# Optimization experiments

Measured on AMD Instinct MI355X. Metric: run time of the kernel, lower is better.

## Reference

```python
import jax, jax.numpy as jnp
import numpy as np

EMBED_DIM = 1024
NUM_HEADS = 16
HEAD_DIM = EMBED_DIM // NUM_HEADS
B, S = 4, 2048


def setup_inputs() -> dict:
    key = jax.random.key(0)
    ks = jax.random.split(key, 9)
    s = 1.0 / np.sqrt(EMBED_DIM)
    x = jax.random.normal(ks[0], (B, S, EMBED_DIM), dtype=jnp.float32)
    # nn.Linear weights stored [out, in]; y = x @ W.T + b
    Wq = jax.random.uniform(ks[1], (EMBED_DIM, EMBED_DIM), jnp.float32, -s, s)
    bq = jax.random.uniform(ks[2], (EMBED_DIM,), jnp.float32, -s, s)
    Wk = jax.random.uniform(ks[3], (EMBED_DIM, EMBED_DIM), jnp.float32, -s, s)
    bk = jax.random.uniform(ks[4], (EMBED_DIM,), jnp.float32, -s, s)
    Wv = jax.random.uniform(ks[5], (EMBED_DIM, EMBED_DIM), jnp.float32, -s, s)
    bv = jax.random.uniform(ks[6], (EMBED_DIM,), jnp.float32, -s, s)
    Wo = jax.random.uniform(ks[7], (EMBED_DIM, EMBED_DIM), jnp.float32, -s, s)
    bo = jax.random.uniform(ks[8], (EMBED_DIM,), jnp.float32, -s, s)
    return {"x": x, "Wq": Wq, "bq": bq, "Wk": Wk, "bk": bk,
            "Wv": Wv, "bv": bv, "Wo": Wo, "bo": bo}


def _split_heads(t):
    b, s, _ = t.shape
    return t.reshape(b, s, NUM_HEADS, HEAD_DIM).transpose(0, 2, 1, 3)  # [B,H,S,D]


def reference(x, Wq, bq, Wk, bk, Wv, bv, Wo, bo):
    q = _split_heads(x @ Wq.T + bq)
    k = _split_heads(x @ Wk.T + bk)
    v = _split_heads(x @ Wv.T + bv)
    scores = jnp.einsum('bhqd,bhkd->bhqk', q, k) / np.sqrt(HEAD_DIM)  # [B,H,S,S]
    attn = jax.nn.softmax(scores, axis=-1)
    ctx = jnp.einsum('bhqk,bhkd->bhqd', attn, v)          # [B,H,S,D]
    ctx = ctx.transpose(0, 2, 1, 3).reshape(x.shape[0], x.shape[1], EMBED_DIM)
    return ctx @ Wo.T + bo
```

## Files before the change

kernel.cpp:

```cpp
#include <hip/hip_runtime.h>
#include <hip/hip_bf16.h>
#include <stdint.h>

typedef __attribute__((ext_vector_type(8))) short  bf16x8;
typedef __attribute__((ext_vector_type(4))) float  f32x4;
typedef __attribute__((ext_vector_type(4))) unsigned int u32x4;
typedef __attribute__((ext_vector_type(2))) unsigned int u32x2;

#define LOG2E 1.4426950408889634f

__device__ __forceinline__ unsigned short f2bf(float f) {
  unsigned int u = __builtin_bit_cast(unsigned int, f);
  u += 0x7fffu + ((u >> 16) & 1u);
  return (unsigned short)(u >> 16);
}

__device__ __forceinline__ unsigned int pk2(float a, float b) {
  __hip_bfloat162 h = __float22bfloat162_rn(make_float2(a, b));
  unsigned int u;
  __builtin_memcpy(&u, &h, 4);
  return u;
}

__device__ __forceinline__ void async16(const void* g, void* l) {
  __builtin_amdgcn_global_load_lds(
      (const __attribute__((address_space(1))) unsigned int*)g,
      (__attribute__((address_space(3))) unsigned int*)l,
      16, 0, 0);
}

__global__ __launch_bounds__(256) void cast_all(
    const float* __restrict__ x,
    const float* __restrict__ Wq, const float* __restrict__ Wk,
    const float* __restrict__ Wv, const float* __restrict__ Wo,
    unsigned short* __restrict__ xb, unsigned short* __restrict__ wqkv,
    unsigned short* __restrict__ wo) {
  int i = blockIdx.x * 256 + threadIdx.x;
  const float* src;
  unsigned short* dst;
  int off;
  if (i < 2097152) {
    src = x; dst = xb; off = i;
  } else {
    int j = i - 2097152;
    int seg = j >> 18; off = j & 262143;
    src = (seg == 0) ? Wq : (seg == 1) ? Wk : (seg == 2) ? Wv : Wo;
    dst = (seg < 3) ? (wqkv + (size_t)seg * 1048576) : wo;
  }
  float4 f = ((const float4*)src)[off];
  uint2 o;
  o.x = pk2(f.x, f.y);
  o.y = pk2(f.z, f.w);
  ((uint2*)dst)[off] = o;
}

__global__ __launch_bounds__(256) void gemm_qkv(
    const unsigned short* __restrict__ xb, const unsigned short* __restrict__ wqkv,
    const float* __restrict__ bq, const float* __restrict__ bk, const float* __restrict__ bv,
    unsigned short* __restrict__ qb, unsigned short* __restrict__ kb,
    unsigned short* __restrict__ vb) {
  __shared__ __align__(16) unsigned short As[128 * 32];
  __shared__ __align__(16) unsigned short Bs[128 * 32];
  __shared__ __align__(16) unsigned short epi[4][64 * 72];
  const int bid = blockIdx.x;
  const int xcd = bid & 7, idx = bid >> 3;
  const int nt = xcd * 3 + (idx % 3);
  const int mt = idx / 3;
  const int m0 = mt * 128, n0 = nt * 128;
  const int tid = threadIdx.x;
  const int wv = tid >> 6, lane = tid & 63, qq = lane >> 4, ln = lane & 15;
  const int wm = wv & 1, wn = wv >> 1;
  const int K = 1024;

  f32x4 acc[4][4];
#pragma unroll
  for (int i = 0; i < 4; ++i)
#pragma unroll
    for (int j = 0; j < 4; ++j) acc[i][j] = f32x4{0.f, 0.f, 0.f, 0.f};

  for (int k0 = 0; k0 < K; k0 += 32) {
#pragma unroll
    for (int i = 0; i < 2; ++i) {
      int cc = wv * 2 + i;
      int jp = cc * 64 + lane;
      int row = jp >> 2, cp = jp & 3;
      int c = cp ^ ((row >> 1) & 3);
      async16(xb   + (size_t)(m0 + row) * K + k0 + c * 8, As + cc * 512);
      async16(wqkv + (size_t)(n0 + row) * K + k0 + c * 8, Bs + cc * 512);
    }
    __syncthreads();
    bf16x8 af[4], bf[4];
#pragma unroll
    for (int i = 0; i < 4; ++i) {
      int row = wm * 64 + i * 16 + ln;
      af[i] = *(const bf16x8*)(As + row * 32 + (qq ^ ((row >> 1) & 3)) * 8);
    }
#pragma unroll
    for (int j = 0; j < 4; ++j) {
      int row = wn * 64 + j * 16 + ln;
      bf[j] = *(const bf16x8*)(Bs + row * 32 + (qq ^ ((row >> 1) & 3)) * 8);
    }
#pragma unroll
    for (int i = 0; i < 4; ++i)
#pragma unroll
      for (int j = 0; j < 4; ++j)
        acc[i][j] = __builtin_amdgcn_mfma_f32_16x16x32_bf16(af[i], bf[j], acc[i][j], 0, 0, 0);
    __syncthreads();
  }

  const int nblk = n0 >> 10;
  const float* bias = (nblk == 0) ? bq : (nblk == 1) ? bk : bv;
  const float scale = (nblk == 0) ? (0.125f * LOG2E) : 1.0f;
  unsigned short* buf = epi[wv];
  const int ncol0 = (n0 & 1023) + wn * 64;
  const int head  = ncol0 >> 6;
  const int mbase = m0 + wm * 64;
  const int b     = mbase >> 11, sbase = mbase & 2047;
  unsigned short* dst = (nblk == 0) ? qb : (nblk == 1) ? kb : vb;

  if (nblk != 2) {
#pragma unroll
    for (int j = 0; j < 4; ++j) {
      float bs = bias[ncol0 + j * 16 + ln] * scale;
#pragma unroll
      for (int i = 0; i < 4; ++i)
#pragma unroll
        for (int r = 0; r < 4; ++r)
          buf[(i * 16 + qq * 4 + r) * 72 + j * 16 + ln] = f2bf(acc[i][j][r] * scale + bs);
    }
    unsigned short* gout = dst + (((size_t)(b * 16 + head)) * 2048 + sbase) * 64;
#pragma unroll
    for (int h = 0; h < 2; ++h)
#pragma unroll
      for (int p = 0; p < 4; ++p) {
        int rr = (lane >> 2) + p * 16;
        int c4 = lane & 3;
        ulonglong2 v = *(const ulonglong2*)(buf + rr * 72 + h * 32 + c4 * 8);
        *(ulonglong2*)(gout + (size_t)rr * 64 + h * 32 + c4 * 8) = v;
      }
  } else {
#pragma unroll
    for (int j = 0; j < 4; ++j) {
      float bs = bias[ncol0 + j * 16 + ln];
#pragma unroll
      for (int i = 0; i < 4; ++i) {
        uint2 pk;
        pk.x = pk2(acc[i][j][0] + bs, acc[i][j][1] + bs);
        pk.y = pk2(acc[i][j][2] + bs, acc[i][j][3] + bs);
        *(uint2*)(buf + (j * 16 + ln) * 72 + i * 16 + qq * 4) = pk;
      }
    }
    unsigned short* gout = dst + ((size_t)(b * 16 + head)) * 64 * 2048 + sbase;
#pragma unroll
    for (int p = 0; p < 8; ++p) {
      int dr = (lane >> 3) + p * 8;
      int c8 = lane & 7;
      ulonglong2 v = *(const ulonglong2*)(buf + dr * 72 + c8 * 8);
      *(ulonglong2*)(gout + (size_t)dr * 2048 + c8 * 8) = v;
    }
  }
}

__global__ __launch_bounds__(256, 2) void attn_kernel(
    const unsigned short* __restrict__ qb, const unsigned short* __restrict__ kb,
    const unsigned short* __restrict__ vb, unsigned short* __restrict__ ctx) {
  __shared__ __align__(16) unsigned short sh[16384];
  const int bid = blockIdx.x;
  const int xcd = bid & 7, idx = bid >> 3;
  const int bh = xcd * 8 + (idx >> 3);
  const int q0 = (idx & 7) * 256;
  const int tid = threadIdx.x;
  const int wv = tid >> 6, lane = tid & 63, qq = lane >> 4, ln = lane & 15;

  bf16x8 qf[4][2];
  {
    const unsigned short* qbase = qb + ((size_t)bh * 2048 + q0 + wv * 64) * 64;
#pragma unroll
    for (int rb = 0; rb < 4; ++rb)
#pragma unroll
      for (int kq = 0; kq < 2; ++kq)
        qf[rb][kq] = *(const bf16x8*)(qbase + (rb * 16 + ln) * 64 + kq * 32 + qq * 8);
  }

  f32x4 o_acc[4][4];
  float l_i[4] = {0.f, 0.f, 0.f, 0.f};
#pragma unroll
  for (int rb = 0; rb < 4; ++rb)
#pragma unroll
    for (int nt = 0; nt < 4; ++nt) o_acc[rb][nt] = f32x4{0.f, 0.f, 0.f, 0.f};
  const f32x4 z4 = f32x4{0.f, 0.f, 0.f, 0.f};

  const unsigned short* kgbase = kb + (size_t)bh * 2048 * 64;
  const unsigned short* vgbase = vb + (size_t)bh * 64 * 2048;
  const int cc0 = wv * 2;

  auto stageKV = [&](int kt, int buf) {
#pragma unroll
    for (int i = 0; i < 2; ++i) {
      int jp = (cc0 + i) * 64 + lane;
      int row = jp >> 3, c = (jp & 7) ^ (row & 7);
      async16(kgbase + (size_t)(kt * 64 + row) * 64 + c * 8,
              sh + buf * 4096 + (cc0 + i) * 512);
      async16(vgbase + (size_t)row * 2048 + kt * 64 + c * 8,
              sh + 8192 + buf * 4096 + (cc0 + i) * 512);
    }
  };

  stageKV(0, 0);
  asm volatile("s_waitcnt vmcnt(0)" ::: "memory");
  __builtin_amdgcn_s_barrier();

  for (int kt = 0; kt < 32; ++kt) {
    const int cur = kt & 1;
    const unsigned short* kcur = sh + cur * 4096;
    const unsigned short* vcur = sh + 8192 + cur * 4096;
    if (kt < 31) stageKV(kt + 1, cur ^ 1);

    bf16x8 kf[4][2];
#pragma unroll
    for (int ct = 0; ct < 4; ++ct) {
      int row = ct * 16 + ln;
      kf[ct][0] = *(const bf16x8*)(kcur + row * 64 + ((0 + qq) ^ (row & 7)) * 8);
      kf[ct][1] = *(const bf16x8*)(kcur + row * 64 + ((4 + qq) ^ (row & 7)) * 8);
    }
    bf16x8 vf[2][4];
#pragma unroll
    for (int kk = 0; kk < 2; ++kk)
#pragma unroll
      for (int nt = 0; nt < 4; ++nt) {
        int row = nt * 16 + ln;
        vf[kk][nt] = *(const bf16x8*)(vcur + row * 64 + ((kk * 4 + qq) ^ (row & 7)) * 8);
      }

    auto QK = [&](const bf16x8& q0f, const bf16x8& q1f, f32x4* s) {
#pragma unroll
      for (int ct = 0; ct < 4; ++ct) {
        s[ct] = __builtin_amdgcn_mfma_f32_16x16x32_bf16(kf[ct][0], q0f, z4, 0, 0, 0);
        s[ct] = __builtin_amdgcn_mfma_f32_16x16x32_bf16(kf[ct][1], q1f, s[ct], 0, 0, 0);
      }
    };
    auto SM = [&](float& li, const f32x4* s, bf16x8* pfo) {
      unsigned int W[4][2];
#pragma unroll
      for (int ct = 0; ct < 4; ++ct) {
        float p0 = __builtin_amdgcn_exp2f(s[ct][0]);
        float p1 = __builtin_amdgcn_exp2f(s[ct][1]);
        float p2 = __builtin_amdgcn_exp2f(s[ct][2]);
        float p3 = __builtin_amdgcn_exp2f(s[ct][3]);
        li += (p0 + p1) + (p2 + p3);
        W[ct][0] = pk2(p0, p1);
        W[ct][1] = pk2(p2, p3);
      }
#pragma unroll
      for (int kk = 0; kk < 2; ++kk) {
        u32x2 a1 = __builtin_amdgcn_permlane32_swap(W[2 * kk][0], W[2 * kk + 1][0], false, false);
        u32x2 a2 = __builtin_amdgcn_permlane16_swap(a1.x, a1.y, false, false);
        u32x2 b1 = __builtin_amdgcn_permlane32_swap(W[2 * kk][1], W[2 * kk + 1][1], false, false);
        u32x2 b2 = __builtin_amdgcn_permlane16_swap(b1.x, b1.y, false, false);
        u32x4 pw = {a2.x, b2.x, a2.y, b2.y};
        pfo[kk] = __builtin_bit_cast(bf16x8, pw);
      }
    };
    auto PV = [&](f32x4* oa, const bf16x8* pfi) {
#pragma unroll
      for (int kk = 0; kk < 2; ++kk)
#pragma unroll
        for (int nt = 0; nt < 4; ++nt)
          oa[nt] = __builtin_amdgcn_mfma_f32_16x16x32_bf16(vf[kk][nt], pfi[kk], oa[nt], 0, 0, 0);
    };

    f32x4 s0[4], s1[4], s2[4], s3[4];
    bf16x8 p0[2], p1[2], p2[2], p3[2];
    QK(qf[0][0], qf[0][1], s0);
    QK(qf[1][0], qf[1][1], s1);  SM(l_i[0], s0, p0);
    QK(qf[2][0], qf[2][1], s2);  SM(l_i[1], s1, p1);  PV(o_acc[0], p0);
    QK(qf[3][0], qf[3][1], s3);  SM(l_i[2], s2, p2);  PV(o_acc[1], p1);
                                 SM(l_i[3], s3, p3);  PV(o_acc[2], p2);
                                                      PV(o_acc[3], p3);

    if (kt < 31) asm volatile("s_waitcnt vmcnt(0)" ::: "memory");
    __builtin_amdgcn_s_barrier();
  }

  unsigned short* ep = sh;
#pragma unroll
  for (int rb = 0; rb < 4; ++rb) {
    l_i[rb] += __shfl_xor(l_i[rb], 16);
    l_i[rb] += __shfl_xor(l_i[rb], 32);
    float inv = 1.0f / l_i[rb];
    int row = wv * 64 + rb * 16 + ln;
    int rs = row & 7;
#pragma unroll
    for (int nt = 0; nt < 4; ++nt) {
      uint2 pk;
      pk.x = pk2(o_acc[rb][nt][0] * inv, o_acc[rb][nt][1] * inv);
      pk.y = pk2(o_acc[rb][nt][2] * inv, o_acc[rb][nt][3] * inv);
      *(uint2*)(ep + row * 64 + (((nt * 2 + (qq >> 1)) ^ rs) << 3) + ((qq & 1) << 2)) = pk;
    }
  }
  {
    const int b = bh >> 4, h = bh & 15;
    int r = tid;
    int rs2 = r & 7;
    size_t gbase = ((size_t)(b * 2048 + q0 + r)) * 1024 + h * 64;
    const unsigned short* lsrc = ep + r * 64;
#pragma unroll
    for (int j = 0; j < 8; ++j)
      *(ulonglong2*)(ctx + gbase + (size_t)j * 8) =
          *(const ulonglong2*)(lsrc + ((j ^ rs2) << 3));
  }
}

__global__ __launch_bounds__(256) void gemm_out(
    const unsigned short* __restrict__ ctx, const unsigned short* __restrict__ wo,
    const float* __restrict__ bo, float* __restrict__ out) {
  __shared__ __align__(16) unsigned short As[2][128 * 32];
  __shared__ __align__(16) unsigned short Bs[2][128 * 32];
  const int bid = blockIdx.x;
  const int n0 = (bid & 7) * 128;
  const int m0 = (bid >> 3) * 128;
  const int tid = threadIdx.x;
  const int wv = tid >> 6, lane = tid & 63, qq = lane >> 4, ln = lane & 15;
  const int wm = wv & 1, wn = wv >> 1;
  const int K = 1024;

  f32x4 acc[4][4];
#pragma unroll
  for (int i = 0; i < 4; ++i)
#pragma unroll
    for (int j = 0; j < 4; ++j) acc[i][j] = f32x4{0.f, 0.f, 0.f, 0.f};

  auto stage = [&](int t, int buf) {
#pragma unroll
    for (int i = 0; i < 2; ++i) {
      int cc = wv * 2 + i;
      int jp = cc * 64 + lane;
      int row = jp >> 2, cp = jp & 3;
      int c = cp ^ ((row >> 1) & 3);
      async16(ctx + (size_t)(m0 + row) * K + t * 32 + c * 8, As[buf] + cc * 512);
      async16(wo  + (size_t)(n0 + row) * K + t * 32 + c * 8, Bs[buf] + cc * 512);
    }
  };

  stage(0, 0);
  for (int t = 0; t < 32; ++t) {
    const int cur = t & 1;
    if (t < 31) {
      stage(t + 1, cur ^ 1);
      asm volatile("s_waitcnt vmcnt(4)" ::: "memory");
    } else {
      asm volatile("s_waitcnt vmcnt(0)" ::: "memory");
    }
    __builtin_amdgcn_s_barrier();

    bf16x8 af[4], bf[4];
#pragma unroll
    for (int i = 0; i < 4; ++i) {
      int row = wm * 64 + i * 16 + ln;
      af[i] = *(const bf16x8*)(As[cur] + row * 32 + (qq ^ ((row >> 1) & 3)) * 8);
    }
#pragma unroll
    for (int j = 0; j < 4; ++j) {
      int row = wn * 64 + j * 16 + ln;
      bf[j] = *(const bf16x8*)(Bs[cur] + row * 32 + (qq ^ ((row >> 1) & 3)) * 8);
    }
#pragma unroll
    for (int i = 0; i < 4; ++i)
#pragma unroll
      for (int j = 0; j < 4; ++j)
        acc[i][j] = __builtin_amdgcn_mfma_f32_16x16x32_bf16(af[i], bf[j], acc[i][j], 0, 0, 0);
    __builtin_amdgcn_s_barrier();
  }

#pragma unroll
  for (int j = 0; j < 4; ++j) {
    int n = n0 + wn * 64 + j * 16 + ln;
    float bsv = bo[n];
#pragma unroll
    for (int i = 0; i < 4; ++i) {
#pragma unroll
      for (int r = 0; r < 4; ++r) {
        int m = m0 + wm * 64 + i * 16 + qq * 4 + r;
        out[(size_t)m * 1024 + n] = acc[i][j][r] + bsv;
      }
    }
  }
}

extern "C" void kernel_launch(void* const* d_in, const int* in_sizes, int n_in,
                              void* d_out, int out_size, void* d_ws, size_t ws_size,
                              hipStream_t stream) {
  const float* x  = (const float*)d_in[0];
  const float* Wq = (const float*)d_in[1];
  const float* bq = (const float*)d_in[2];
  const float* Wk = (const float*)d_in[3];
  const float* bk = (const float*)d_in[4];
  const float* Wv = (const float*)d_in[5];
  const float* bv = (const float*)d_in[6];
  const float* Wo = (const float*)d_in[7];
  const float* bo = (const float*)d_in[8];
  float* out = (float*)d_out;

  char* ws = (char*)d_ws;
  unsigned short* xb   = (unsigned short*)(ws);
  unsigned short* ctxb = (unsigned short*)(ws);
  unsigned short* qb   = (unsigned short*)(ws + ((size_t)16 << 20));
  unsigned short* kbuf = (unsigned short*)(ws + ((size_t)32 << 20));
  unsigned short* vbuf = (unsigned short*)(ws + ((size_t)48 << 20));
  unsigned short* wqkv = (unsigned short*)(ws + ((size_t)64 << 20));
  unsigned short* wo   = (unsigned short*)(ws + ((size_t)70 << 20));

  cast_all<<<12288, 256, 0, stream>>>(x, Wq, Wk, Wv, Wo, xb, wqkv, wo);

  gemm_qkv<<<1536, 256, 0, stream>>>(xb, wqkv, bq, bk, bv, qb, kbuf, vbuf);
  attn_kernel<<<512, 256, 0, stream>>>(qb, kbuf, vbuf, ctxb);
  gemm_out<<<512, 256, 0, stream>>>(ctxb, wo, bo, out);
}
```

Measured before the change: 286.5 us.

## Double-buffer QKV GEMM, reuse LDS for swizzled epilogue, shrink output GEMM tile

```diff
diff --git a/kernel.cpp b/kernel.cpp
--- a/kernel.cpp
+++ b/kernel.cpp
@@ -59,9 +59,7 @@
     const float* __restrict__ bq, const float* __restrict__ bk, const float* __restrict__ bv,
     unsigned short* __restrict__ qb, unsigned short* __restrict__ kb,
     unsigned short* __restrict__ vb) {
-  __shared__ __align__(16) unsigned short As[128 * 32];
-  __shared__ __align__(16) unsigned short Bs[128 * 32];
-  __shared__ __align__(16) unsigned short epi[4][64 * 72];
+  __shared__ __align__(16) unsigned short sh[16384];
   const int bid = blockIdx.x;
   const int xcd = bid & 7, idx = bid >> 3;
   const int nt = xcd * 3 + (idx % 3);
@@ -78,40 +76,54 @@
 #pragma unroll
     for (int j = 0; j < 4; ++j) acc[i][j] = f32x4{0.f, 0.f, 0.f, 0.f};
 
-  for (int k0 = 0; k0 < K; k0 += 32) {
+  auto stage = [&](int k0, int buf) {
 #pragma unroll
     for (int i = 0; i < 2; ++i) {
       int cc = wv * 2 + i;
       int jp = cc * 64 + lane;
       int row = jp >> 2, cp = jp & 3;
       int c = cp ^ ((row >> 1) & 3);
-      async16(xb   + (size_t)(m0 + row) * K + k0 + c * 8, As + cc * 512);
-      async16(wqkv + (size_t)(n0 + row) * K + k0 + c * 8, Bs + cc * 512);
-    }
-    __syncthreads();
+      async16(xb   + (size_t)(m0 + row) * K + k0 + c * 8, sh + buf * 4096 + cc * 512);
+      async16(wqkv + (size_t)(n0 + row) * K + k0 + c * 8, sh + 8192 + buf * 4096 + cc * 512);
+    }
+  };
+
+  stage(0, 0);
+  for (int t = 0; t < 32; ++t) {
+    const int cur = t & 1;
+    if (t < 31) {
+      stage((t + 1) * 32, cur ^ 1);
+      asm volatile("s_waitcnt vmcnt(4)" ::: "memory");
+    } else {
+      asm volatile("s_waitcnt vmcnt(0)" ::: "memory");
+    }
+    __builtin_amdgcn_s_barrier();
+
+    const unsigned short* Asb = sh + cur * 4096;
+    const unsigned short* Bsb = sh + 8192 + cur * 4096;
     bf16x8 af[4], bf[4];
 #pragma unroll
     for (int i = 0; i < 4; ++i) {
       int row = wm * 64 + i * 16 + ln;
-      af[i] = *(const bf16x8*)(As + row * 32 + (qq ^ ((row >> 1) & 3)) * 8);
+      af[i] = *(const bf16x8*)(Asb + row * 32 + (qq ^ ((row >> 1) & 3)) * 8);
     }
 #pragma unroll
     for (int j = 0; j < 4; ++j) {
       int row = wn * 64 + j * 16 + ln;
-      bf[j] = *(const bf16x8*)(Bs + row * 32 + (qq ^ ((row >> 1) & 3)) * 8);
+      bf[j] = *(const bf16x8*)(Bsb + row * 32 + (qq ^ ((row >> 1) & 3)) * 8);
     }
 #pragma unroll
     for (int i = 0; i < 4; ++i)
 #pragma unroll
       for (int j = 0; j < 4; ++j)
         acc[i][j] = __builtin_amdgcn_mfma_f32_16x16x32_bf16(af[i], bf[j], acc[i][j], 0, 0, 0);
-    __syncthreads();
+    __builtin_amdgcn_s_barrier();
   }
 
   const int nblk = n0 >> 10;
   const float* bias = (nblk == 0) ? bq : (nblk == 1) ? bk : bv;
   const float scale = (nblk == 0) ? (0.125f * LOG2E) : 1.0f;
-  unsigned short* buf = epi[wv];
+  unsigned short* ep = sh + wv * 4096;
   const int ncol0 = (n0 & 1023) + wn * 64;
   const int head  = ncol0 >> 6;
   const int mbase = m0 + wm * 64;
@@ -122,11 +134,14 @@
 #pragma unroll
     for (int j = 0; j < 4; ++j) {
       float bs = bias[ncol0 + j * 16 + ln] * scale;
+      int csl = j * 2 + (ln >> 3), c7 = ln & 7;
 #pragma unroll
       for (int i = 0; i < 4; ++i)
 #pragma unroll
-        for (int r = 0; r < 4; ++r)
-          buf[(i * 16 + qq * 4 + r) * 72 + j * 16 + ln] = f2bf(acc[i][j][r] * scale + bs);
+        for (int r = 0; r < 4; ++r) {
+          int row = i * 16 + qq * 4 + r;
+          ep[row * 64 + ((csl ^ (row & 7)) << 3) + c7] = f2bf(acc[i][j][r] * scale + bs);
+        }
     }
     unsigned short* gout = dst + (((size_t)(b * 16 + head)) * 2048 + sbase) * 64;
 #pragma unroll
@@ -135,19 +150,22 @@
       for (int p = 0; p < 4; ++p) {
         int rr = (lane >> 2) + p * 16;
         int c4 = lane & 3;
-        ulonglong2 v = *(const ulonglong2*)(buf + rr * 72 + h * 32 + c4 * 8);
+        ulonglong2 v = *(const ulonglong2*)(ep + rr * 64 + (((h * 4 + c4) ^ (rr & 7)) << 3));
         *(ulonglong2*)(gout + (size_t)rr * 64 + h * 32 + c4 * 8) = v;
       }
   } else {
 #pragma unroll
     for (int j = 0; j < 4; ++j) {
       float bs = bias[ncol0 + j * 16 + ln];
+      int row = j * 16 + ln;
+      int rs = row & 7;
 #pragma unroll
       for (int i = 0; i < 4; ++i) {
         uint2 pk;
         pk.x = pk2(acc[i][j][0] + bs, acc[i][j][1] + bs);
         pk.y = pk2(acc[i][j][2] + bs, acc[i][j][3] + bs);
-        *(uint2*)(buf + (j * 16 + ln) * 72 + i * 16 + qq * 4) = pk;
+        int slot = (i * 2 + (qq >> 1)) ^ rs;
+        *(uint2*)(ep + row * 64 + (slot << 3) + ((qq & 1) << 2)) = pk;
       }
     }
     unsigned short* gout = dst + ((size_t)(b * 16 + head)) * 64 * 2048 + sbase;
@@ -155,7 +173,7 @@
     for (int p = 0; p < 8; ++p) {
       int dr = (lane >> 3) + p * 8;
       int c8 = lane & 7;
-      ulonglong2 v = *(const ulonglong2*)(buf + dr * 72 + c8 * 8);
+      ulonglong2 v = *(const ulonglong2*)(ep + dr * 64 + ((c8 ^ (dr & 7)) << 3));
       *(ulonglong2*)(gout + (size_t)dr * 2048 + c8 * 8) = v;
     }
   }
@@ -311,34 +329,38 @@
   }
 }
 
-__global__ __launch_bounds__(256) void gemm_out(
+__global__ __launch_bounds__(256, 4) void gemm_out(
     const unsigned short* __restrict__ ctx, const unsigned short* __restrict__ wo,
     const float* __restrict__ bo, float* __restrict__ out) {
-  __shared__ __align__(16) unsigned short As[2][128 * 32];
-  __shared__ __align__(16) unsigned short Bs[2][128 * 32];
+  __shared__ __align__(16) unsigned short Asd[2][64 * 32];
+  __shared__ __align__(16) unsigned short Bsd[2][128 * 32];
   const int bid = blockIdx.x;
   const int n0 = (bid & 7) * 128;
-  const int m0 = (bid >> 3) * 128;
+  const int m0 = (bid >> 3) * 64;
   const int tid = threadIdx.x;
   const int wv = tid >> 6, lane = tid & 63, qq = lane >> 4, ln = lane & 15;
-  const int wm = wv & 1, wn = wv >> 1;
   const int K = 1024;
 
-  f32x4 acc[4][4];
+  f32x4 acc[4][2];
 #pragma unroll
   for (int i = 0; i < 4; ++i)
 #pragma unroll
-    for (int j = 0; j < 4; ++j) acc[i][j] = f32x4{0.f, 0.f, 0.f, 0.f};
+    for (int j = 0; j < 2; ++j) acc[i][j] = f32x4{0.f, 0.f, 0.f, 0.f};
 
   auto stage = [&](int t, int buf) {
+    {
+      int jp = wv * 64 + lane;
+      int row = jp >> 2, cp = jp & 3;
+      int c = cp ^ ((row >> 1) & 3);
+      async16(ctx + (size_t)(m0 + row) * K + t * 32 + c * 8, Asd[buf] + wv * 512);
+    }
 #pragma unroll
     for (int i = 0; i < 2; ++i) {
       int cc = wv * 2 + i;
       int jp = cc * 64 + lane;
       int row = jp >> 2, cp = jp & 3;
       int c = cp ^ ((row >> 1) & 3);
-      async16(ctx + (size_t)(m0 + row) * K + t * 32 + c * 8, As[buf] + cc * 512);
-      async16(wo  + (size_t)(n0 + row) * K + t * 32 + c * 8, Bs[buf] + cc * 512);
+      async16(wo + (size_t)(n0 + row) * K + t * 32 + c * 8, Bsd[buf] + cc * 512);
     }
   };
 
@@ -347,40 +369,40 @@
     const int cur = t & 1;
     if (t < 31) {
       stage(t + 1, cur ^ 1);
-      asm volatile("s_waitcnt vmcnt(4)" ::: "memory");
+      asm volatile("s_waitcnt vmcnt(3)" ::: "memory");
     } else {
       asm volatile("s_waitcnt vmcnt(0)" ::: "memory");
     }
     __builtin_amdgcn_s_barrier();
 
-    bf16x8 af[4], bf[4];
+    bf16x8 af[4], bf[2];
 #pragma unroll
     for (int i = 0; i < 4; ++i) {
-      int row = wm * 64 + i * 16 + ln;
-      af[i] = *(const bf16x8*)(As[cur] + row * 32 + (qq ^ ((row >> 1) & 3)) * 8);
-    }
-#pragma unroll
-    for (int j = 0; j < 4; ++j) {
-      int row = wn * 64 + j * 16 + ln;
-      bf[j] = *(const bf16x8*)(Bs[cur] + row * 32 + (qq ^ ((row >> 1) & 3)) * 8);
+      int row = i * 16 + ln;
+      af[i] = *(const bf16x8*)(Asd[cur] + row * 32 + (qq ^ ((row >> 1) & 3)) * 8);
+    }
+#pragma unroll
+    for (int j = 0; j < 2; ++j) {
+      int row = wv * 32 + j * 16 + ln;
+      bf[j] = *(const bf16x8*)(Bsd[cur] + row * 32 + (qq ^ ((row >> 1) & 3)) * 8);
     }
 #pragma unroll
     for (int i = 0; i < 4; ++i)
 #pragma unroll
-      for (int j = 0; j < 4; ++j)
+      for (int j = 0; j < 2; ++j)
         acc[i][j] = __builtin_amdgcn_mfma_f32_16x16x32_bf16(af[i], bf[j], acc[i][j], 0, 0, 0);
     __builtin_amdgcn_s_barrier();
   }
 
 #pragma unroll
-  for (int j = 0; j < 4; ++j) {
-    int n = n0 + wn * 64 + j * 16 + ln;
+  for (int j = 0; j < 2; ++j) {
+    int n = n0 + wv * 32 + j * 16 + ln;
     float bsv = bo[n];
 #pragma unroll
     for (int i = 0; i < 4; ++i) {
 #pragma unroll
       for (int r = 0; r < 4; ++r) {
-        int m = m0 + wm * 64 + i * 16 + qq * 4 + r;
+        int m = m0 + i * 16 + qq * 4 + r;
         out[(size_t)m * 1024 + n] = acc[i][j][r] + bsv;
       }
     }
@@ -414,5 +436,5 @@
 
   gemm_qkv<<<1536, 256, 0, stream>>>(xb, wqkv, bq, bk, bv, qb, kbuf, vbuf);
   attn_kernel<<<512, 256, 0, stream>>>(qb, kbuf, vbuf, ctxb);
-  gemm_out<<<512, 256, 0, stream>>>(ctxb, wo, bo, out);
-}
+  gemm_out<<<1024, 256, 0, stream>>>(ctxb, wo, bo, out);
+}
```

Result: no change. 282.0 us (-1.6%).
